# Optimization experiments

Hardware: AMD Instinct MI355X
Metric: run time of the kernel (lower is better)

The kernel has to match this reference:

```python
import jax, jax.numpy as jnp
import numpy as np

D_MODEL = 2048
N_HEADS = 16
D_K = D_MODEL // N_HEADS  # 128


def setup_inputs() -> dict:
    key = jax.random.key(0)
    ks = jax.random.split(key, 12)
    B, S = 2, 2048
    std = 1.0 / np.sqrt(D_MODEL)
    inp = {
        "query": jax.random.normal(ks[0], (B, S, D_MODEL), jnp.float32),
        "key": jax.random.normal(ks[1], (B, S, D_MODEL), jnp.float32),
        "value": jax.random.normal(ks[2], (B, S, D_MODEL), jnp.float32),
        "w_q": jax.random.normal(ks[3], (D_MODEL, D_MODEL), jnp.float32) * std,
        "b_q": jnp.zeros((D_MODEL,), jnp.float32),
        "w_k": jax.random.normal(ks[4], (D_MODEL, D_MODEL), jnp.float32) * std,
        "b_k": jnp.zeros((D_MODEL,), jnp.float32),
        "w_v": jax.random.normal(ks[5], (D_MODEL, D_MODEL), jnp.float32) * std,
        "b_v": jnp.zeros((D_MODEL,), jnp.float32),
        "w_o": jax.random.normal(ks[6], (D_MODEL, D_MODEL), jnp.float32) * std,
        "b_o": jnp.zeros((D_MODEL,), jnp.float32),
        # fractional scale numerator / denominator per head; ratio ~ 1/sqrt(d_k)
        "scale_alpha": jnp.full((N_HEADS,), 1.0, jnp.float32),
        "scale_beta": jnp.full((N_HEADS,), float(np.sqrt(D_K)), jnp.float32),
    }
    return inp


def reference(query, key, value, w_q, b_q, w_k, b_k, w_v, b_v, w_o, b_o,
              scale_alpha, scale_beta):
    B, S, _ = query.shape
    # projections (torch Linear: x @ W^T + b)
    Q = (query @ w_q.T + b_q).reshape(B, S, N_HEADS, D_K).transpose(0, 2, 1, 3)
    K = (key @ w_k.T + b_k).reshape(B, S, N_HEADS, D_K).transpose(0, 2, 1, 3)
    V = (value @ w_v.T + b_v).reshape(B, S, N_HEADS, D_K).transpose(0, 2, 1, 3)
    # per-head fractional scale alpha/beta (computed under no_grad in torch)
    scales = jax.lax.stop_gradient(scale_alpha / jnp.maximum(scale_beta, 1.0))
    scores = jnp.einsum("bhqd,bhkd->bhqk", Q, K) * scales[None, :, None, None]
    attn = jax.nn.softmax(scores, axis=-1)  # dropout is identity in eval
    out = jnp.einsum("bhqk,bhkd->bhqd", attn, V)
    out = out.transpose(0, 2, 1, 3).reshape(B, S, D_MODEL)
    return out @ w_o.T + b_o
```

## Files before the change

kernel.cpp:

```cpp
#include <hip/hip_runtime.h>
#include <cstdint>

#define S_LEN   2048
#define DMODEL  2048
#define NHEADS  16
#define DK      128
#define MROWS   4096

typedef _Float16 f16;
using f16x8 = __attribute__((ext_vector_type(8))) _Float16;
using f16x4 = __attribute__((ext_vector_type(4))) _Float16;
using f32x4 = __attribute__((ext_vector_type(4))) float;

typedef const __attribute__((address_space(1))) unsigned int gu32;
typedef __attribute__((address_space(3))) unsigned int lu32;

__device__ __forceinline__ void gl2lds16(const void* g, void* l) {
    __builtin_amdgcn_global_load_lds((gu32*)g, (lu32*)l, 16, 0, 0);
}

__global__ __launch_bounds__(256) void cvt_all(
    const float* __restrict__ q, const float* __restrict__ k,
    const float* __restrict__ v, const float* __restrict__ wq,
    const float* __restrict__ wk, const float* __restrict__ wv,
    const float* __restrict__ wo,
    f16* cq, f16* ck, f16* cv, f16* cwq, f16* cwk, f16* cwv, f16* cwo)
{
    const int b = blockIdx.x;
    const float* src; f16* dst; int base;
    if      (b <  8192) { src = q;  dst = cq;  base = b; }
    else if (b < 16384) { src = k;  dst = ck;  base = b - 8192; }
    else if (b < 24576) { src = v;  dst = cv;  base = b - 16384; }
    else if (b < 28672) { src = wq; dst = cwq; base = b - 24576; }
    else if (b < 32768) { src = wk; dst = cwk; base = b - 28672; }
    else if (b < 36864) { src = wv; dst = cwv; base = b - 32768; }
    else                { src = wo; dst = cwo; base = b - 36864; }
    const int i = base * 256 + threadIdx.x;
    float4 x = ((const float4*)src)[i];
    f16x4 o; o[0] = (f16)x.x; o[1] = (f16)x.y; o[2] = (f16)x.z; o[3] = (f16)x.w;
    ((f16x4*)dst)[i] = o;
}

__device__ __forceinline__ void gemm_core(
    const f16* __restrict__ A, const f16* __restrict__ W,
    const float* __restrict__ bias, void* __restrict__ Cout,
    int mode, const float* __restrict__ sa, const float* __restrict__ sb)
{
    __shared__ f16 As[128 * 32];
    __shared__ f16 Bs[128 * 32];

    const int tid = threadIdx.x;
    const int bm = blockIdx.y * 128;
    const int bn = blockIdx.x * 128;
    const int wid = tid >> 6;
    const int ln = tid & 15;
    const int quad = (tid & 63) >> 4;
    const int wm = (wid >> 1) * 64;
    const int wn = (wid & 1) * 64;
    const int K = DMODEL, N = DMODEL;

    f32x4 acc[4][4];
#pragma unroll
    for (int i = 0; i < 4; ++i)
#pragma unroll
        for (int j = 0; j < 4; ++j)
            acc[i][j] = (f32x4){0.f, 0.f, 0.f, 0.f};

    const int sr = tid >> 2;
    const int ke = (tid & 3) * 8;
    const f16* ga0 = A + (size_t)(bm + sr) * K + ke;
    const f16* ga1 = A + (size_t)(bm + 64 + sr) * K + ke;
    const f16* gb0 = W + (size_t)(bn + sr) * K + ke;
    const f16* gb1 = W + (size_t)(bn + 64 + sr) * K + ke;
    f16* la0 = As + tid * 8;
    f16* la1 = As + 2048 + tid * 8;
    f16* lb0 = Bs + tid * 8;
    f16* lb1 = Bs + 2048 + tid * 8;

    for (int k0 = 0; k0 < K; k0 += 32) {
        __syncthreads();
        gl2lds16(ga0 + k0, la0);
        gl2lds16(ga1 + k0, la1);
        gl2lds16(gb0 + k0, lb0);
        gl2lds16(gb1 + k0, lb1);
        __syncthreads();

        f16x8 af[4], bf[4];
#pragma unroll
        for (int i = 0; i < 4; ++i)
            af[i] = *(const f16x8*)&As[(wm + i * 16 + ln) * 32 + quad * 8];
#pragma unroll
        for (int j = 0; j < 4; ++j)
            bf[j] = *(const f16x8*)&Bs[(wn + j * 16 + ln) * 32 + quad * 8];
#pragma unroll
        for (int i = 0; i < 4; ++i)
#pragma unroll
            for (int j = 0; j < 4; ++j)
                acc[i][j] = __builtin_amdgcn_mfma_f32_16x16x32_f16(
                    af[i], bf[j], acc[i][j], 0, 0, 0);
    }

#pragma unroll
    for (int j = 0; j < 4; ++j) {
        const int n = bn + wn + j * 16 + ln;
        const float bn_ = bias[n];
        const int h = n >> 7;
        const int d = n & (DK - 1);
        float scq = 1.0f;
        if (mode == 3) scq = sa[h] / fmaxf(sb[h], 1.0f);
#pragma unroll
        for (int i = 0; i < 4; ++i) {
#pragma unroll
            for (int reg = 0; reg < 4; ++reg) {
                const int m = bm + wm + i * 16 + quad * 4 + reg;
                float v = acc[i][j][reg] + bn_;
                if (mode == 0) {
                    ((float*)Cout)[(size_t)m * N + n] = v;
                } else {
                    const int bb = m >> 11;
                    const int ss = m & (S_LEN - 1);
                    size_t idx;
                    if (mode == 2)
                        idx = (((size_t)(bb * NHEADS + h) * DK + d) * S_LEN + ss);
                    else
                        idx = (((size_t)(bb * NHEADS + h) * S_LEN + ss) * DK + d);
                    if (mode == 3) v *= scq;
                    ((f16*)Cout)[idx] = (f16)v;
                }
            }
        }
    }
}

__global__ __launch_bounds__(256) void qkv_gemm(
    const f16* Aq, const f16* Ak, const f16* Av,
    const f16* Wq, const f16* Wk, const f16* Wv,
    const float* bq, const float* bk, const float* bv,
    f16* Oq, f16* Ok, f16* Ov, const float* sa, const float* sb)
{
    const int z = blockIdx.z;
    const f16* A = (z == 0) ? Aq : (z == 1) ? Ak : Av;
    const f16* W = (z == 0) ? Wq : (z == 1) ? Wk : Wv;
    const float* bias = (z == 0) ? bq : (z == 1) ? bk : bv;
    void* O = (z == 0) ? (void*)Oq : (z == 1) ? (void*)Ok : (void*)Ov;
    const int mode = (z == 0) ? 3 : (z == 1) ? 1 : 2;
    gemm_core(A, W, bias, O, mode, sa, sb);
}

__global__ __launch_bounds__(256) void out_gemm(
    const f16* A, const f16* W, const float* bias, float* O)
{
    gemm_core(A, W, bias, O, 0, nullptr, nullptr);
}

__global__ __launch_bounds__(256, 2) void flash_v4(
    const f16* __restrict__ Qg, const f16* __restrict__ Kg,
    const f16* __restrict__ VTg, f16* __restrict__ AO)
{
    __shared__ f16 Ks[4 * 64 * 32];
    __shared__ f16 Vs[2 * 128 * 32];
    __shared__ f16 Ps[2 * 128 * 32];
    __shared__ float l_buf[2 * 128];

    const int tid = threadIdx.x;
    const int wid = tid >> 6;
    const int ln = tid & 15;
    const int quad = (tid & 63) >> 4;
    const int wq = wid & 1;
    const int wc = wid >> 1;
    const int bh = blockIdx.y;
    const int q0 = blockIdx.x * 128;

    f16x8 qf[4][4];
    const f16* Qbase = Qg + ((size_t)bh * S_LEN + q0 + wq * 64) * DK;
#pragma unroll
    for (int nt = 0; nt < 4; ++nt)
#pragma unroll
        for (int kc = 0; kc < 4; ++kc)
            qf[nt][kc] = *(const f16x8*)(Qbase + (size_t)(nt * 16 + ln) * DK
                                         + kc * 32 + quad * 8);

    f32x4 o[4][4];
    float lp[4] = {0.f, 0.f, 0.f, 0.f};
#pragma unroll
    for (int i = 0; i < 4; ++i)
#pragma unroll
        for (int j = 0; j < 4; ++j)
            o[i][j] = (f32x4){0.f, 0.f, 0.f, 0.f};

    const f16* Kgb = Kg + (size_t)bh * S_LEN * DK;
    const f16* Vgb = VTg + (size_t)bh * DK * S_LEN;
    const int srow = tid >> 2;
    const int soff = (tid & 3) * 8;

    for (int kt = 0; kt < S_LEN / 64; ++kt) {
        __syncthreads();
#pragma unroll
        for (int j = 0; j < 4; ++j)
            gl2lds16(Kgb + (size_t)(kt * 64 + srow) * DK + j * 32 + soff,
                     Ks + j * 2048 + tid * 8);
#pragma unroll
        for (int j = 0; j < 4; ++j)
            gl2lds16(Vgb + (size_t)(srow + (j & 1) * 64) * S_LEN
                         + kt * 64 + (j >> 1) * 32 + soff,
                     Vs + (j >> 1) * 4096 + (j & 1) * 2048 + tid * 8);
        __syncthreads();

        f32x4 s[2][4];
#pragma unroll
        for (int mt = 0; mt < 2; ++mt)
#pragma unroll
            for (int nt = 0; nt < 4; ++nt)
                s[mt][nt] = (f32x4){0.f, 0.f, 0.f, 0.f};
#pragma unroll
        for (int kc = 0; kc < 4; ++kc) {
            f16x8 kf0 = *(const f16x8*)&Ks[kc * 2048 + (wc * 32 + ln) * 32 + quad * 8];
            f16x8 kf1 = *(const f16x8*)&Ks[kc * 2048 + (wc * 32 + 16 + ln) * 32 + quad * 8];
#pragma unroll
            for (int nt = 0; nt < 4; ++nt) {
                s[0][nt] = __builtin_amdgcn_mfma_f32_16x16x32_f16(kf0, qf[nt][kc], s[0][nt], 0, 0, 0);
                s[1][nt] = __builtin_amdgcn_mfma_f32_16x16x32_f16(kf1, qf[nt][kc], s[1][nt], 0, 0, 0);
            }
        }

#pragma unroll
        for (int mt = 0; mt < 2; ++mt) {
#pragma unroll
            for (int nt = 0; nt < 4; ++nt) {
                const float p0 = __expf(s[mt][nt][0]);
                const float p1 = __expf(s[mt][nt][1]);
                const float p2 = __expf(s[mt][nt][2]);
                const float p3 = __expf(s[mt][nt][3]);
                lp[nt] += (p0 + p1) + (p2 + p3);
                f16x4 pk;
                pk[0] = (f16)p0; pk[1] = (f16)p1; pk[2] = (f16)p2; pk[3] = (f16)p3;
                *(f16x4*)&Ps[wc * 4096 + (wq * 64 + nt * 16 + ln) * 32
                             + mt * 16 + quad * 4] = pk;
            }
        }
        __syncthreads();

#pragma unroll
        for (int cc = 0; cc < 2; ++cc) {
            f16x8 pf[4];
#pragma unroll
            for (int mtq = 0; mtq < 4; ++mtq)
                pf[mtq] = *(const f16x8*)&Ps[cc * 4096 + (wq * 64 + mtq * 16 + ln) * 32 + quad * 8];
#pragma unroll
            for (int ntd = 0; ntd < 4; ++ntd) {
                f16x8 vf = *(const f16x8*)&Vs[cc * 4096 + (wc * 64 + ntd * 16 + ln) * 32 + quad * 8];
#pragma unroll
                for (int mtq = 0; mtq < 4; ++mtq)
                    o[mtq][ntd] = __builtin_amdgcn_mfma_f32_16x16x32_f16(
                        pf[mtq], vf, o[mtq][ntd], 0, 0, 0);
            }
        }
    }

#pragma unroll
    for (int nt = 0; nt < 4; ++nt) {
        float v = lp[nt];
        v += __shfl_xor(v, 16, 64);
        v += __shfl_xor(v, 32, 64);
        lp[nt] = v;
    }
    if (quad == 0) {
#pragma unroll
        for (int nt = 0; nt < 4; ++nt)
            l_buf[wc * 128 + wq * 64 + nt * 16 + ln] = lp[nt];
    }
    __syncthreads();

    const int b = bh >> 4;
    const int h = bh & (NHEADS - 1);
#pragma unroll
    for (int mtq = 0; mtq < 4; ++mtq) {
#pragma unroll
        for (int reg = 0; reg < 4; ++reg) {
            const int ql = wq * 64 + mtq * 16 + quad * 4 + reg;
            const float inv = 1.0f / (l_buf[ql] + l_buf[128 + ql]);
            f16* dst = AO + ((size_t)b * S_LEN + q0 + ql) * DMODEL + h * DK + wc * 64;
#pragma unroll
            for (int ntd = 0; ntd < 4; ++ntd)
                dst[ntd * 16 + ln] = (f16)(o[mtq][ntd][reg] * inv);
        }
    }
}

extern "C" void kernel_launch(void* const* d_in, const int* in_sizes, int n_in,
                              void* d_out, int out_size, void* d_ws, size_t ws_size,
                              hipStream_t stream)
{
    (void)in_sizes; (void)n_in; (void)out_size; (void)ws_size;
    const float* query = (const float*)d_in[0];
    const float* key_  = (const float*)d_in[1];
    const float* value = (const float*)d_in[2];
    const float* w_q = (const float*)d_in[3];
    const float* b_q = (const float*)d_in[4];
    const float* w_k = (const float*)d_in[5];
    const float* b_k = (const float*)d_in[6];
    const float* w_v = (const float*)d_in[7];
    const float* b_v = (const float*)d_in[8];
    const float* w_o = (const float*)d_in[9];
    const float* b_o = (const float*)d_in[10];
    const float* s_alpha = (const float*)d_in[11];
    const float* s_beta  = (const float*)d_in[12];
    float* out = (float*)d_out;

    const size_t T = (size_t)MROWS * DMODEL;
    const size_t Wn = (size_t)DMODEL * DMODEL;
    f16* base = (f16*)d_ws;
    f16* c_q = base;
    f16* c_k = base + T;
    f16* c_v = base + 2 * T;
    f16* Qh  = base + 3 * T;
    f16* wq16 = base + 4 * T;
    f16* wk16 = wq16 + Wn;
    f16* wv16 = wk16 + Wn;
    f16* wo16 = wv16 + Wn;
    f16* Kh  = c_q;
    f16* VT  = c_k;
    f16* AOh = c_v;

    dim3 blk(256);

    cvt_all<<<dim3(40960), blk, 0, stream>>>(query, key_, value, w_q, w_k, w_v, w_o,
                                             c_q, c_k, c_v, wq16, wk16, wv16, wo16);

    dim3 qkv_grid(DMODEL / 128, MROWS / 128, 3);
    qkv_gemm<<<qkv_grid, blk, 0, stream>>>(c_q, c_k, c_v, wq16, wk16, wv16,
                                           b_q, b_k, b_v, Qh, Kh, VT,
                                           s_alpha, s_beta);

    dim3 flash_grid(S_LEN / 128, 2 * NHEADS);
    flash_v4<<<flash_grid, blk, 0, stream>>>(Qh, Kh, VT, AOh);

    dim3 out_grid(DMODEL / 128, MROWS / 128);
    out_gemm<<<out_grid, blk, 0, stream>>>(AOh, wo16, b_o, out);
}
```

Before: 489.1 us.

## Triple-buffer GEMM with swizzled LDS, 128x256 tiles, and grid-stride conversion

The projection GEMMs move to 512-thread blocks with 128x256 tiles and a three-stage LDS ring. Global-to-LDS loads for tile t+2 are issued while MFMAs on tile t run, gated by vmcnt waits and raw barriers, and the compute phases get raised wave priority. An XOR swizzle on the K-chunk offset is meant to reduce LDS bank conflicts. The fp32-to-fp16 conversion kernel becomes a grid-stride loop over 2048 blocks instead of one block per chunk. The larger tiles and buffers raise LDS and register use and halve the block count, which may reduce occupancy. The hand-counted vmcnt synchronization is fragile.

```diff
diff --git a/kernel.cpp b/kernel.cpp
--- a/kernel.cpp
+++ b/kernel.cpp
@@ -19,6 +19,7 @@
     __builtin_amdgcn_global_load_lds((gu32*)g, (lu32*)l, 16, 0, 0);
 }
 
+#define CVT_BLOCKS 2048
 __global__ __launch_bounds__(256) void cvt_all(
     const float* __restrict__ q, const float* __restrict__ k,
     const float* __restrict__ v, const float* __restrict__ wq,
@@ -26,37 +27,44 @@
     const float* __restrict__ wo,
     f16* cq, f16* ck, f16* cv, f16* cwq, f16* cwk, f16* cwv, f16* cwo)
 {
-    const int b = blockIdx.x;
-    const float* src; f16* dst; int base;
-    if      (b <  8192) { src = q;  dst = cq;  base = b; }
-    else if (b < 16384) { src = k;  dst = ck;  base = b - 8192; }
-    else if (b < 24576) { src = v;  dst = cv;  base = b - 16384; }
-    else if (b < 28672) { src = wq; dst = cwq; base = b - 24576; }
-    else if (b < 32768) { src = wk; dst = cwk; base = b - 28672; }
-    else if (b < 36864) { src = wv; dst = cwv; base = b - 32768; }
-    else                { src = wo; dst = cwo; base = b - 36864; }
-    const int i = base * 256 + threadIdx.x;
-    float4 x = ((const float4*)src)[i];
-    f16x4 o; o[0] = (f16)x.x; o[1] = (f16)x.y; o[2] = (f16)x.z; o[3] = (f16)x.w;
-    ((f16x4*)dst)[i] = o;
-}
+    const unsigned QS = 2097152u;
+    const unsigned WS = 1048576u;
+    const unsigned total = 3u * QS + 4u * WS;
+    unsigned i = blockIdx.x * 256 + threadIdx.x;
+    const unsigned stride = CVT_BLOCKS * 256;
+    for (; i < total; i += stride) {
+        const float* src; f16* dst; unsigned off;
+        if      (i < QS)              { src = q;  dst = cq;  off = i; }
+        else if (i < 2u*QS)           { src = k;  dst = ck;  off = i - QS; }
+        else if (i < 3u*QS)           { src = v;  dst = cv;  off = i - 2u*QS; }
+        else if (i < 3u*QS + WS)      { src = wq; dst = cwq; off = i - 3u*QS; }
+        else if (i < 3u*QS + 2u*WS)   { src = wk; dst = cwk; off = i - (3u*QS + WS); }
+        else if (i < 3u*QS + 3u*WS)   { src = wv; dst = cwv; off = i - (3u*QS + 2u*WS); }
+        else                          { src = wo; dst = cwo; off = i - (3u*QS + 3u*WS); }
+        float4 x = ((const float4*)src)[off];
+        f16x4 o; o[0] = (f16)x.x; o[1] = (f16)x.y; o[2] = (f16)x.z; o[3] = (f16)x.w;
+        ((f16x4*)dst)[off] = o;
+    }
+}
+
+#define NT_K (DMODEL / 32)
 
 __device__ __forceinline__ void gemm_core(
     const f16* __restrict__ A, const f16* __restrict__ W,
     const float* __restrict__ bias, void* __restrict__ Cout,
     int mode, const float* __restrict__ sa, const float* __restrict__ sb)
 {
-    __shared__ f16 As[128 * 32];
-    __shared__ f16 Bs[128 * 32];
+    __shared__ f16 As[3][128 * 32];
+    __shared__ f16 Bs[3][256 * 32];
 
     const int tid = threadIdx.x;
-    const int bm = blockIdx.y * 128;
-    const int bn = blockIdx.x * 128;
     const int wid = tid >> 6;
     const int ln = tid & 15;
     const int quad = (tid & 63) >> 4;
-    const int wm = (wid >> 1) * 64;
-    const int wn = (wid & 1) * 64;
+    const int wm = (wid >> 2) * 64;
+    const int wn = (wid & 3) * 64;
+    const int bm = blockIdx.y * 128;
+    const int bn = blockIdx.x * 256;
     const int K = DMODEL, N = DMODEL;
 
     f32x4 acc[4][4];
@@ -67,37 +75,67 @@
             acc[i][j] = (f32x4){0.f, 0.f, 0.f, 0.f};
 
     const int sr = tid >> 2;
-    const int ke = (tid & 3) * 8;
-    const f16* ga0 = A + (size_t)(bm + sr) * K + ke;
-    const f16* ga1 = A + (size_t)(bm + 64 + sr) * K + ke;
-    const f16* gb0 = W + (size_t)(bn + sr) * K + ke;
-    const f16* gb1 = W + (size_t)(bn + 64 + sr) * K + ke;
-    f16* la0 = As + tid * 8;
-    f16* la1 = As + 2048 + tid * 8;
-    f16* lb0 = Bs + tid * 8;
-    f16* lb1 = Bs + 2048 + tid * 8;
-
-    for (int k0 = 0; k0 < K; k0 += 32) {
-        __syncthreads();
-        gl2lds16(ga0 + k0, la0);
-        gl2lds16(ga1 + k0, la1);
-        gl2lds16(gb0 + k0, lb0);
-        gl2lds16(gb1 + k0, lb1);
-        __syncthreads();
-
-        f16x8 af[4], bf[4];
-#pragma unroll
-        for (int i = 0; i < 4; ++i)
-            af[i] = *(const f16x8*)&As[(wm + i * 16 + ln) * 32 + quad * 8];
-#pragma unroll
-        for (int j = 0; j < 4; ++j)
-            bf[j] = *(const f16x8*)&Bs[(wn + j * 16 + ln) * 32 + quad * 8];
-#pragma unroll
-        for (int i = 0; i < 4; ++i)
+    const int kcs = ((tid & 3) ^ ((tid >> 3) & 3)) * 8;
+    const f16* gA  = A + (size_t)(bm + sr) * K + kcs;
+    const f16* gB0 = W + (size_t)(bn + sr) * K + kcs;
+    const f16* gB1 = W + (size_t)(bn + 128 + sr) * K + kcs;
+    const int koff = (quad ^ ((ln >> 1) & 3)) * 8;
+
+    gl2lds16(gA,        &As[0][tid * 8]);
+    gl2lds16(gB0,       &Bs[0][tid * 8]);
+    gl2lds16(gB1,       &Bs[0][4096 + tid * 8]);
+    gl2lds16(gA  + 32,  &As[1][tid * 8]);
+    gl2lds16(gB0 + 32,  &Bs[1][tid * 8]);
+    gl2lds16(gB1 + 32,  &Bs[1][4096 + tid * 8]);
+
+    for (int t = 0; t < NT_K; ++t) {
+        const f16* Ab = As[t % 3];
+        const f16* Bb = Bs[t % 3];
+        if (t < NT_K - 1) asm volatile("s_waitcnt vmcnt(3)" ::: "memory");
+        else              asm volatile("s_waitcnt vmcnt(0)" ::: "memory");
+        __builtin_amdgcn_s_barrier();
+
+        f16x8 af[2], bf[4];
+#pragma unroll
+        for (int i = 0; i < 2; ++i)
+            af[i] = *(const f16x8*)&Ab[(wm + i * 16 + ln) * 32 + koff];
+#pragma unroll
+        for (int j = 0; j < 4; ++j)
+            bf[j] = *(const f16x8*)&Bb[(wn + j * 16 + ln) * 32 + koff];
+        if (t + 2 < NT_K) {
+            const int b2 = (t + 2) % 3;
+            const int k2 = (t + 2) * 32;
+            gl2lds16(gA  + k2, &As[b2][tid * 8]);
+            gl2lds16(gB0 + k2, &Bs[b2][tid * 8]);
+        }
+        __builtin_amdgcn_s_barrier();
+        __builtin_amdgcn_s_setprio(1);
+#pragma unroll
+        for (int i = 0; i < 2; ++i)
 #pragma unroll
             for (int j = 0; j < 4; ++j)
                 acc[i][j] = __builtin_amdgcn_mfma_f32_16x16x32_f16(
                     af[i], bf[j], acc[i][j], 0, 0, 0);
+        __builtin_amdgcn_s_setprio(0);
+        __builtin_amdgcn_s_barrier();
+
+#pragma unroll
+        for (int i = 0; i < 2; ++i)
+            af[i] = *(const f16x8*)&Ab[(wm + (2 + i) * 16 + ln) * 32 + koff];
+        if (t + 2 < NT_K) {
+            const int b2 = (t + 2) % 3;
+            const int k2 = (t + 2) * 32;
+            gl2lds16(gB1 + k2, &Bs[b2][4096 + tid * 8]);
+        }
+        __builtin_amdgcn_s_barrier();
+        __builtin_amdgcn_s_setprio(1);
+#pragma unroll
+        for (int i = 0; i < 2; ++i)
+#pragma unroll
+            for (int j = 0; j < 4; ++j)
+                acc[2 + i][j] = __builtin_amdgcn_mfma_f32_16x16x32_f16(
+                    af[i], bf[j], acc[2 + i][j], 0, 0, 0);
+        __builtin_amdgcn_s_setprio(0);
     }
 
 #pragma unroll
@@ -132,7 +170,7 @@
     }
 }
 
-__global__ __launch_bounds__(256) void qkv_gemm(
+__global__ __launch_bounds__(512, 2) void qkv_gemm(
     const f16* Aq, const f16* Ak, const f16* Av,
     const f16* Wq, const f16* Wk, const f16* Wv,
     const float* bq, const float* bk, const float* bv,
@@ -147,7 +185,7 @@
     gemm_core(A, W, bias, O, mode, sa, sb);
 }
 
-__global__ __launch_bounds__(256) void out_gemm(
+__global__ __launch_bounds__(512, 2) void out_gemm(
     const f16* A, const f16* W, const float* bias, float* O)
 {
     gemm_core(A, W, bias, O, 0, nullptr, nullptr);
@@ -322,19 +360,18 @@
     f16* VT  = c_k;
     f16* AOh = c_v;
 
-    dim3 blk(256);
-
-    cvt_all<<<dim3(40960), blk, 0, stream>>>(query, key_, value, w_q, w_k, w_v, w_o,
-                                             c_q, c_k, c_v, wq16, wk16, wv16, wo16);
-
-    dim3 qkv_grid(DMODEL / 128, MROWS / 128, 3);
-    qkv_gemm<<<qkv_grid, blk, 0, stream>>>(c_q, c_k, c_v, wq16, wk16, wv16,
-                                           b_q, b_k, b_v, Qh, Kh, VT,
-                                           s_alpha, s_beta);
+    cvt_all<<<dim3(CVT_BLOCKS), dim3(256), 0, stream>>>(
+        query, key_, value, w_q, w_k, w_v, w_o,
+        c_q, c_k, c_v, wq16, wk16, wv16, wo16);
+
+    dim3 qkv_grid(DMODEL / 256, MROWS / 128, 3);
+    qkv_gemm<<<qkv_grid, dim3(512), 0, stream>>>(c_q, c_k, c_v, wq16, wk16, wv16,
+                                                 b_q, b_k, b_v, Qh, Kh, VT,
+                                                 s_alpha, s_beta);
 
     dim3 flash_grid(S_LEN / 128, 2 * NHEADS);
-    flash_v4<<<flash_grid, blk, 0, stream>>>(Qh, Kh, VT, AOh);
-
-    dim3 out_grid(DMODEL / 128, MROWS / 128);
-    out_gemm<<<out_grid, blk, 0, stream>>>(AOh, wo16, b_o, out);
-}
+    flash_v4<<<flash_grid, dim3(256), 0, stream>>>(Qh, Kh, VT, AOh);
+
+    dim3 out_grid(DMODEL / 256, MROWS / 128);
+    out_gemm<<<out_grid, dim3(512), 0, stream>>>(AOh, wo16, b_o, out);
+}
```

Measured after the change: 498.2 us. Within noise of the previous version (+1.9%).

## Use 256-row GEMM tiles with 4-stage async LDS pipeline and swizzled LDS

Applied to the files above, without the earlier changes.

Replaces the 128x128 single-buffered GEMM with 512-thread blocks computing 256x256 tiles (QKV) or 256x128 tiles (output projection). Global-to-LDS loads now run through a 4-deep ring buffer with explicit vmcnt waits and MFMA priority raising. Both the GEMM and the flash-attention K, V and P tiles get an XOR swizzle on the LDS layout to avoid bank conflicts. K and V^T are moved into the output buffer so the QKV GEMM no longer overwrites its own input buffers while other blocks still read them. The larger tiles and deeper buffering use more LDS and registers, which may limit occupancy.

```diff
diff --git a/kernel.cpp b/kernel.cpp
--- a/kernel.cpp
+++ b/kernel.cpp
@@ -41,67 +41,108 @@
     ((f16x4*)dst)[i] = o;
 }
 
-__device__ __forceinline__ void gemm_core(
+#define NT_K (DMODEL / 32)
+
+template<int BN>
+__device__ __forceinline__ void gemm_core2(
     const f16* __restrict__ A, const f16* __restrict__ W,
     const float* __restrict__ bias, void* __restrict__ Cout,
     int mode, const float* __restrict__ sa, const float* __restrict__ sb)
 {
-    __shared__ f16 As[128 * 32];
-    __shared__ f16 Bs[128 * 32];
-
-    const int tid = threadIdx.x;
-    const int bm = blockIdx.y * 128;
-    const int bn = blockIdx.x * 128;
-    const int wid = tid >> 6;
-    const int ln = tid & 15;
+    constexpr int NJ = BN / 64;
+    __shared__ f16 As[4][256 * 32];
+    __shared__ f16 Bs[4][BN * 32];
+
+    const int tid  = threadIdx.x;
+    const int wid  = tid >> 6;
+    const int ln   = tid & 15;
     const int quad = (tid & 63) >> 4;
-    const int wm = (wid >> 1) * 64;
-    const int wn = (wid & 1) * 64;
+    const int wm   = (wid >> 2) * 128;
+    const int wn   = (wid & 3) * (16 * NJ);
+    const int bm   = blockIdx.y * 256;
+    const int bn   = blockIdx.x * BN;
     const int K = DMODEL, N = DMODEL;
 
-    f32x4 acc[4][4];
-#pragma unroll
-    for (int i = 0; i < 4; ++i)
-#pragma unroll
-        for (int j = 0; j < 4; ++j)
+    f32x4 acc[8][NJ];
+#pragma unroll
+    for (int i = 0; i < 8; ++i)
+#pragma unroll
+        for (int j = 0; j < NJ; ++j)
             acc[i][j] = (f32x4){0.f, 0.f, 0.f, 0.f};
 
-    const int sr = tid >> 2;
-    const int ke = (tid & 3) * 8;
-    const f16* ga0 = A + (size_t)(bm + sr) * K + ke;
-    const f16* ga1 = A + (size_t)(bm + 64 + sr) * K + ke;
-    const f16* gb0 = W + (size_t)(bn + sr) * K + ke;
-    const f16* gb1 = W + (size_t)(bn + 64 + sr) * K + ke;
-    f16* la0 = As + tid * 8;
-    f16* la1 = As + 2048 + tid * 8;
-    f16* lb0 = Bs + tid * 8;
-    f16* lb1 = Bs + 2048 + tid * 8;
-
-    for (int k0 = 0; k0 < K; k0 += 32) {
-        __syncthreads();
-        gl2lds16(ga0 + k0, la0);
-        gl2lds16(ga1 + k0, la1);
-        gl2lds16(gb0 + k0, lb0);
-        gl2lds16(gb1 + k0, lb1);
-        __syncthreads();
-
-        f16x8 af[4], bf[4];
+    const int sr  = tid >> 2;
+    const int kcs = ((tid & 3) ^ ((tid >> 3) & 3)) * 8;
+    const f16* gA0 = A + (size_t)(bm + sr) * K + kcs;
+    const f16* gA1 = A + (size_t)(bm + 128 + sr) * K + kcs;
+    const f16* gB0 = W + (size_t)(bn + sr) * K + kcs;
+    const f16* gB1 = W + (size_t)(bn + 128 + sr) * K + kcs;
+    const int koff = (quad ^ ((ln >> 1) & 3)) * 8;
+
+#define STAGE_A(t_) do { const int b_ = (t_) & 3; const int k_ = (t_) * 32; \
+        gl2lds16(gA0 + k_, &As[b_][tid * 8]);                               \
+        gl2lds16(gA1 + k_, &As[b_][4096 + tid * 8]); } while (0)
+#define STAGE_B(t_) do { const int b_ = (t_) & 3; const int k_ = (t_) * 32; \
+        gl2lds16(gB0 + k_, &Bs[b_][tid * 8]);                               \
+        if (BN == 256) gl2lds16(gB1 + k_, &Bs[b_][4096 + tid * 8]); } while (0)
+
+    STAGE_A(0); STAGE_B(0);
+    STAGE_A(1); STAGE_B(1);
+    STAGE_A(2); STAGE_B(2);
+
+    for (int t = 0; t < NT_K; ++t) {
+        const f16* Ab = As[t & 3];
+        const f16* Bb = Bs[t & 3];
+        if (BN == 256) {
+            if (t < NT_K - 2)       asm volatile("s_waitcnt vmcnt(8)" ::: "memory");
+            else if (t == NT_K - 2) asm volatile("s_waitcnt vmcnt(4)" ::: "memory");
+            else                    asm volatile("s_waitcnt vmcnt(0)" ::: "memory");
+        } else {
+            if (t < NT_K - 2)       asm volatile("s_waitcnt vmcnt(6)" ::: "memory");
+            else if (t == NT_K - 2) asm volatile("s_waitcnt vmcnt(3)" ::: "memory");
+            else                    asm volatile("s_waitcnt vmcnt(0)" ::: "memory");
+        }
+        __builtin_amdgcn_s_barrier();
+        __builtin_amdgcn_sched_barrier(0);
+
+        f16x8 af[4], bf[NJ];
 #pragma unroll
         for (int i = 0; i < 4; ++i)
-            af[i] = *(const f16x8*)&As[(wm + i * 16 + ln) * 32 + quad * 8];
-#pragma unroll
-        for (int j = 0; j < 4; ++j)
-            bf[j] = *(const f16x8*)&Bs[(wn + j * 16 + ln) * 32 + quad * 8];
+            af[i] = *(const f16x8*)&Ab[(wm + i * 16 + ln) * 32 + koff];
+#pragma unroll
+        for (int j = 0; j < NJ; ++j)
+            bf[j] = *(const f16x8*)&Bb[(wn + j * 16 + ln) * 32 + koff];
+        if (t + 3 < NT_K) STAGE_A(t + 3);
+        asm volatile("s_waitcnt lgkmcnt(0)" ::: "memory");
+        __builtin_amdgcn_sched_barrier(0);
+        __builtin_amdgcn_s_setprio(1);
 #pragma unroll
         for (int i = 0; i < 4; ++i)
 #pragma unroll
-            for (int j = 0; j < 4; ++j)
+            for (int j = 0; j < NJ; ++j)
                 acc[i][j] = __builtin_amdgcn_mfma_f32_16x16x32_f16(
                     af[i], bf[j], acc[i][j], 0, 0, 0);
-    }
-
-#pragma unroll
-    for (int j = 0; j < 4; ++j) {
+        __builtin_amdgcn_s_setprio(0);
+
+#pragma unroll
+        for (int i = 0; i < 4; ++i)
+            af[i] = *(const f16x8*)&Ab[(wm + (4 + i) * 16 + ln) * 32 + koff];
+        if (t + 3 < NT_K) STAGE_B(t + 3);
+        asm volatile("s_waitcnt lgkmcnt(0)" ::: "memory");
+        __builtin_amdgcn_sched_barrier(0);
+        __builtin_amdgcn_s_setprio(1);
+#pragma unroll
+        for (int i = 0; i < 4; ++i)
+#pragma unroll
+            for (int j = 0; j < NJ; ++j)
+                acc[4 + i][j] = __builtin_amdgcn_mfma_f32_16x16x32_f16(
+                    af[i], bf[j], acc[4 + i][j], 0, 0, 0);
+        __builtin_amdgcn_s_setprio(0);
+    }
+#undef STAGE_A
+#undef STAGE_B
+
+#pragma unroll
+    for (int j = 0; j < NJ; ++j) {
         const int n = bn + wn + j * 16 + ln;
         const float bn_ = bias[n];
         const int h = n >> 7;
@@ -109,7 +150,7 @@
         float scq = 1.0f;
         if (mode == 3) scq = sa[h] / fmaxf(sb[h], 1.0f);
 #pragma unroll
-        for (int i = 0; i < 4; ++i) {
+        for (int i = 0; i < 8; ++i) {
 #pragma unroll
             for (int reg = 0; reg < 4; ++reg) {
                 const int m = bm + wm + i * 16 + quad * 4 + reg;
@@ -132,7 +173,7 @@
     }
 }
 
-__global__ __launch_bounds__(256) void qkv_gemm(
+__global__ __launch_bounds__(512, 2) void qkv_gemm(
     const f16* Aq, const f16* Ak, const f16* Av,
     const f16* Wq, const f16* Wk, const f16* Wv,
     const float* bq, const float* bk, const float* bv,
@@ -144,13 +185,13 @@
     const float* bias = (z == 0) ? bq : (z == 1) ? bk : bv;
     void* O = (z == 0) ? (void*)Oq : (z == 1) ? (void*)Ok : (void*)Ov;
     const int mode = (z == 0) ? 3 : (z == 1) ? 1 : 2;
-    gemm_core(A, W, bias, O, mode, sa, sb);
-}
-
-__global__ __launch_bounds__(256) void out_gemm(
+    gemm_core2<256>(A, W, bias, O, mode, sa, sb);
+}
+
+__global__ __launch_bounds__(512, 2) void out_gemm(
     const f16* A, const f16* W, const float* bias, float* O)
 {
-    gemm_core(A, W, bias, O, 0, nullptr, nullptr);
+    gemm_core2<128>(A, W, bias, O, 0, nullptr, nullptr);
 }
 
 __global__ __launch_bounds__(256, 2) void flash_v4(
@@ -171,6 +212,9 @@
     const int bh = blockIdx.y;
     const int q0 = blockIdx.x * 128;
 
+    const int koff = (quad ^ ((ln >> 1) & 3)) * 8;
+    const int soff_sw = ((tid & 3) ^ ((tid >> 3) & 3)) * 8;
+
     f16x8 qf[4][4];
     const f16* Qbase = Qg + ((size_t)bh * S_LEN + q0 + wq * 64) * DK;
 #pragma unroll
@@ -191,18 +235,17 @@
     const f16* Kgb = Kg + (size_t)bh * S_LEN * DK;
     const f16* Vgb = VTg + (size_t)bh * DK * S_LEN;
     const int srow = tid >> 2;
-    const int soff = (tid & 3) * 8;
 
     for (int kt = 0; kt < S_LEN / 64; ++kt) {
         __syncthreads();
 #pragma unroll
         for (int j = 0; j < 4; ++j)
-            gl2lds16(Kgb + (size_t)(kt * 64 + srow) * DK + j * 32 + soff,
+            gl2lds16(Kgb + (size_t)(kt * 64 + srow) * DK + j * 32 + soff_sw,
                      Ks + j * 2048 + tid * 8);
 #pragma unroll
         for (int j = 0; j < 4; ++j)
             gl2lds16(Vgb + (size_t)(srow + (j & 1) * 64) * S_LEN
-                         + kt * 64 + (j >> 1) * 32 + soff,
+                         + kt * 64 + (j >> 1) * 32 + soff_sw,
                      Vs + (j >> 1) * 4096 + (j & 1) * 2048 + tid * 8);
         __syncthreads();
 
@@ -212,16 +255,18 @@
 #pragma unroll
             for (int nt = 0; nt < 4; ++nt)
                 s[mt][nt] = (f32x4){0.f, 0.f, 0.f, 0.f};
+        __builtin_amdgcn_s_setprio(1);
 #pragma unroll
         for (int kc = 0; kc < 4; ++kc) {
-            f16x8 kf0 = *(const f16x8*)&Ks[kc * 2048 + (wc * 32 + ln) * 32 + quad * 8];
-            f16x8 kf1 = *(const f16x8*)&Ks[kc * 2048 + (wc * 32 + 16 + ln) * 32 + quad * 8];
+            f16x8 kf0 = *(const f16x8*)&Ks[kc * 2048 + (wc * 32 + ln) * 32 + koff];
+            f16x8 kf1 = *(const f16x8*)&Ks[kc * 2048 + (wc * 32 + 16 + ln) * 32 + koff];
 #pragma unroll
             for (int nt = 0; nt < 4; ++nt) {
                 s[0][nt] = __builtin_amdgcn_mfma_f32_16x16x32_f16(kf0, qf[nt][kc], s[0][nt], 0, 0, 0);
                 s[1][nt] = __builtin_amdgcn_mfma_f32_16x16x32_f16(kf1, qf[nt][kc], s[1][nt], 0, 0, 0);
             }
         }
+        __builtin_amdgcn_s_setprio(0);
 
 #pragma unroll
         for (int mt = 0; mt < 2; ++mt) {
@@ -234,27 +279,30 @@
                 lp[nt] += (p0 + p1) + (p2 + p3);
                 f16x4 pk;
                 pk[0] = (f16)p0; pk[1] = (f16)p1; pk[2] = (f16)p2; pk[3] = (f16)p3;
-                *(f16x4*)&Ps[wc * 4096 + (wq * 64 + nt * 16 + ln) * 32
-                             + mt * 16 + quad * 4] = pk;
+                const int pchunk = ((mt * 2 + (quad >> 1)) ^ ((ln >> 1) & 3)) * 8
+                                   + (quad & 1) * 4;
+                *(f16x4*)&Ps[wc * 4096 + (wq * 64 + nt * 16 + ln) * 32 + pchunk] = pk;
             }
         }
         __syncthreads();
 
+        __builtin_amdgcn_s_setprio(1);
 #pragma unroll
         for (int cc = 0; cc < 2; ++cc) {
             f16x8 pf[4];
 #pragma unroll
             for (int mtq = 0; mtq < 4; ++mtq)
-                pf[mtq] = *(const f16x8*)&Ps[cc * 4096 + (wq * 64 + mtq * 16 + ln) * 32 + quad * 8];
+                pf[mtq] = *(const f16x8*)&Ps[cc * 4096 + (wq * 64 + mtq * 16 + ln) * 32 + koff];
 #pragma unroll
             for (int ntd = 0; ntd < 4; ++ntd) {
-                f16x8 vf = *(const f16x8*)&Vs[cc * 4096 + (wc * 64 + ntd * 16 + ln) * 32 + quad * 8];
+                f16x8 vf = *(const f16x8*)&Vs[cc * 4096 + (wc * 64 + ntd * 16 + ln) * 32 + koff];
 #pragma unroll
                 for (int mtq = 0; mtq < 4; ++mtq)
                     o[mtq][ntd] = __builtin_amdgcn_mfma_f32_16x16x32_f16(
                         pf[mtq], vf, o[mtq][ntd], 0, 0, 0);
             }
         }
+        __builtin_amdgcn_s_setprio(0);
     }
 
 #pragma unroll
@@ -318,23 +366,22 @@
     f16* wk16 = wq16 + Wn;
     f16* wv16 = wk16 + Wn;
     f16* wo16 = wv16 + Wn;
-    f16* Kh  = c_q;
-    f16* VT  = c_k;
+    f16* Kh  = (f16*)d_out;
+    f16* VT  = Kh + T;
     f16* AOh = c_v;
 
-    dim3 blk(256);
-
-    cvt_all<<<dim3(40960), blk, 0, stream>>>(query, key_, value, w_q, w_k, w_v, w_o,
-                                             c_q, c_k, c_v, wq16, wk16, wv16, wo16);
-
-    dim3 qkv_grid(DMODEL / 128, MROWS / 128, 3);
-    qkv_gemm<<<qkv_grid, blk, 0, stream>>>(c_q, c_k, c_v, wq16, wk16, wv16,
-                                           b_q, b_k, b_v, Qh, Kh, VT,
-                                           s_alpha, s_beta);
+    cvt_all<<<dim3(40960), dim3(256), 0, stream>>>(
+        query, key_, value, w_q, w_k, w_v, w_o,
+        c_q, c_k, c_v, wq16, wk16, wv16, wo16);
+
+    dim3 qkv_grid(DMODEL / 256, MROWS / 256, 3);
+    qkv_gemm<<<qkv_grid, dim3(512), 0, stream>>>(c_q, c_k, c_v, wq16, wk16, wv16,
+                                                 b_q, b_k, b_v, Qh, Kh, VT,
+                                                 s_alpha, s_beta);
 
     dim3 flash_grid(S_LEN / 128, 2 * NHEADS);
-    flash_v4<<<flash_grid, blk, 0, stream>>>(Qh, Kh, VT, AOh);
-
-    dim3 out_grid(DMODEL / 128, MROWS / 128);
-    out_gemm<<<out_grid, blk, 0, stream>>>(AOh, wo16, b_o, out);
-}
+    flash_v4<<<flash_grid, dim3(256), 0, stream>>>(Qh, Kh, VT, AOh);
+
+    dim3 out_grid(DMODEL / 128, MROWS / 256);
+    out_gemm<<<out_grid, dim3(512), 0, stream>>>(AOh, wo16, b_o, out);
+}
```

Measured after the change: 484.3 us. About the same (-1.0%).

## Double-buffer K tiles, swizzle LDS layouts, and remap blocks in flash attention

Applied to the files above, without the earlier changes.

The flash kernel now double-buffers K tiles in LDS: the next K tile is prefetched while the current scores and softmax are computed, and explicit waitcnt plus s_barrier replace the full __syncthreads. K, V and P in LDS use an XOR-swizzled chunk layout to reduce bank conflicts. Block indices are remapped to group work for better L2 locality, and s_setprio is raised around the MFMA sections. The fp32-to-fp16 conversion kernel does four vectors per thread. K and V^T scratch moves into the output buffer, which also removes aliasing with the converted query that qkv_gemm is still reading. The hand-written wait counts are fragile if the load order ever changes.

```diff
diff --git a/kernel.cpp b/kernel.cpp
--- a/kernel.cpp
+++ b/kernel.cpp
@@ -28,17 +28,20 @@
 {
     const int b = blockIdx.x;
     const float* src; f16* dst; int base;
-    if      (b <  8192) { src = q;  dst = cq;  base = b; }
-    else if (b < 16384) { src = k;  dst = ck;  base = b - 8192; }
-    else if (b < 24576) { src = v;  dst = cv;  base = b - 16384; }
-    else if (b < 28672) { src = wq; dst = cwq; base = b - 24576; }
-    else if (b < 32768) { src = wk; dst = cwk; base = b - 28672; }
-    else if (b < 36864) { src = wv; dst = cwv; base = b - 32768; }
-    else                { src = wo; dst = cwo; base = b - 36864; }
-    const int i = base * 256 + threadIdx.x;
-    float4 x = ((const float4*)src)[i];
-    f16x4 o; o[0] = (f16)x.x; o[1] = (f16)x.y; o[2] = (f16)x.z; o[3] = (f16)x.w;
-    ((f16x4*)dst)[i] = o;
+    if      (b <  2048) { src = q;  dst = cq;  base = b; }
+    else if (b <  4096) { src = k;  dst = ck;  base = b - 2048; }
+    else if (b <  6144) { src = v;  dst = cv;  base = b - 4096; }
+    else if (b <  7168) { src = wq; dst = cwq; base = b - 6144; }
+    else if (b <  8192) { src = wk; dst = cwk; base = b - 7168; }
+    else if (b <  9216) { src = wv; dst = cwv; base = b - 8192; }
+    else                { src = wo; dst = cwo; base = b - 9216; }
+    const int i = base * 1024 + threadIdx.x;
+#pragma unroll
+    for (int u = 0; u < 4; ++u) {
+        float4 x = ((const float4*)src)[i + u * 256];
+        f16x4 o; o[0] = (f16)x.x; o[1] = (f16)x.y; o[2] = (f16)x.z; o[3] = (f16)x.w;
+        ((f16x4*)dst)[i + u * 256] = o;
+    }
 }
 
 __device__ __forceinline__ void gemm_core(
@@ -153,11 +156,11 @@
     gemm_core(A, W, bias, O, 0, nullptr, nullptr);
 }
 
-__global__ __launch_bounds__(256, 2) void flash_v4(
+__global__ __launch_bounds__(256, 2) void flash_v6(
     const f16* __restrict__ Qg, const f16* __restrict__ Kg,
     const f16* __restrict__ VTg, f16* __restrict__ AO)
 {
-    __shared__ f16 Ks[4 * 64 * 32];
+    __shared__ f16 Ks[2][4 * 64 * 32];
     __shared__ f16 Vs[2 * 128 * 32];
     __shared__ f16 Ps[2 * 128 * 32];
     __shared__ float l_buf[2 * 128];
@@ -168,8 +171,14 @@
     const int quad = (tid & 63) >> 4;
     const int wq = wid & 1;
     const int wc = wid >> 1;
-    const int bh = blockIdx.y;
-    const int q0 = blockIdx.x * 128;
+
+    const int lin = blockIdx.x + (blockIdx.y << 4);
+    const int swz = (lin & 7) * 64 + (lin >> 3);
+    const int q0 = (swz & 15) * 128;
+    const int bh = swz >> 4;
+
+    const int koff = (quad ^ ((ln >> 1) & 3)) * 8;
+    const int soff_sw = ((tid & 3) ^ ((tid >> 3) & 3)) * 8;
 
     f16x8 qf[4][4];
     const f16* Qbase = Qg + ((size_t)bh * S_LEN + q0 + wq * 64) * DK;
@@ -191,36 +200,52 @@
     const f16* Kgb = Kg + (size_t)bh * S_LEN * DK;
     const f16* Vgb = VTg + (size_t)bh * DK * S_LEN;
     const int srow = tid >> 2;
-    const int soff = (tid & 3) * 8;
+
+#pragma unroll
+    for (int j = 0; j < 4; ++j)
+        gl2lds16(Kgb + (size_t)(srow)*DK + j * 32 + soff_sw,
+                 &Ks[0][j * 2048 + tid * 8]);
 
     for (int kt = 0; kt < S_LEN / 64; ++kt) {
-        __syncthreads();
-#pragma unroll
-        for (int j = 0; j < 4; ++j)
-            gl2lds16(Kgb + (size_t)(kt * 64 + srow) * DK + j * 32 + soff,
-                     Ks + j * 2048 + tid * 8);
+        asm volatile("s_waitcnt lgkmcnt(0)" ::: "memory");
+        __builtin_amdgcn_s_barrier();
+        __builtin_amdgcn_sched_barrier(0);
+
 #pragma unroll
         for (int j = 0; j < 4; ++j)
             gl2lds16(Vgb + (size_t)(srow + (j & 1) * 64) * S_LEN
-                         + kt * 64 + (j >> 1) * 32 + soff,
+                         + kt * 64 + (j >> 1) * 32 + soff_sw,
                      Vs + (j >> 1) * 4096 + (j & 1) * 2048 + tid * 8);
-        __syncthreads();
-
+
+        asm volatile("s_waitcnt vmcnt(4)" ::: "memory");
+        __builtin_amdgcn_s_barrier();
+        __builtin_amdgcn_sched_barrier(0);
+
+        const f16* Kb = &Ks[kt & 1][0];
         f32x4 s[2][4];
 #pragma unroll
         for (int mt = 0; mt < 2; ++mt)
 #pragma unroll
             for (int nt = 0; nt < 4; ++nt)
                 s[mt][nt] = (f32x4){0.f, 0.f, 0.f, 0.f};
+        __builtin_amdgcn_s_setprio(1);
 #pragma unroll
         for (int kc = 0; kc < 4; ++kc) {
-            f16x8 kf0 = *(const f16x8*)&Ks[kc * 2048 + (wc * 32 + ln) * 32 + quad * 8];
-            f16x8 kf1 = *(const f16x8*)&Ks[kc * 2048 + (wc * 32 + 16 + ln) * 32 + quad * 8];
+            f16x8 kf0 = *(const f16x8*)&Kb[kc * 2048 + (wc * 32 + ln) * 32 + koff];
+            f16x8 kf1 = *(const f16x8*)&Kb[kc * 2048 + (wc * 32 + 16 + ln) * 32 + koff];
 #pragma unroll
             for (int nt = 0; nt < 4; ++nt) {
                 s[0][nt] = __builtin_amdgcn_mfma_f32_16x16x32_f16(kf0, qf[nt][kc], s[0][nt], 0, 0, 0);
                 s[1][nt] = __builtin_amdgcn_mfma_f32_16x16x32_f16(kf1, qf[nt][kc], s[1][nt], 0, 0, 0);
             }
+        }
+        __builtin_amdgcn_s_setprio(0);
+
+        if (kt + 1 < S_LEN / 64) {
+#pragma unroll
+            for (int j = 0; j < 4; ++j)
+                gl2lds16(Kgb + (size_t)((kt + 1) * 64 + srow) * DK + j * 32 + soff_sw,
+                         &Ks[(kt + 1) & 1][j * 2048 + tid * 8]);
         }
 
 #pragma unroll
@@ -234,27 +259,35 @@
                 lp[nt] += (p0 + p1) + (p2 + p3);
                 f16x4 pk;
                 pk[0] = (f16)p0; pk[1] = (f16)p1; pk[2] = (f16)p2; pk[3] = (f16)p3;
-                *(f16x4*)&Ps[wc * 4096 + (wq * 64 + nt * 16 + ln) * 32
-                             + mt * 16 + quad * 4] = pk;
+                const int pchunk = ((mt * 2 + (quad >> 1)) ^ ((ln >> 1) & 3)) * 8
+                                   + (quad & 1) * 4;
+                *(f16x4*)&Ps[wc * 4096 + (wq * 64 + nt * 16 + ln) * 32 + pchunk] = pk;
             }
         }
-        __syncthreads();
-
+
+        if (kt + 1 < S_LEN / 64) asm volatile("s_waitcnt vmcnt(4)" ::: "memory");
+        else                     asm volatile("s_waitcnt vmcnt(0)" ::: "memory");
+        asm volatile("s_waitcnt lgkmcnt(0)" ::: "memory");
+        __builtin_amdgcn_s_barrier();
+        __builtin_amdgcn_sched_barrier(0);
+
+        __builtin_amdgcn_s_setprio(1);
 #pragma unroll
         for (int cc = 0; cc < 2; ++cc) {
             f16x8 pf[4];
 #pragma unroll
             for (int mtq = 0; mtq < 4; ++mtq)
-                pf[mtq] = *(const f16x8*)&Ps[cc * 4096 + (wq * 64 + mtq * 16 + ln) * 32 + quad * 8];
+                pf[mtq] = *(const f16x8*)&Ps[cc * 4096 + (wq * 64 + mtq * 16 + ln) * 32 + koff];
 #pragma unroll
             for (int ntd = 0; ntd < 4; ++ntd) {
-                f16x8 vf = *(const f16x8*)&Vs[cc * 4096 + (wc * 64 + ntd * 16 + ln) * 32 + quad * 8];
+                f16x8 vf = *(const f16x8*)&Vs[cc * 4096 + (wc * 64 + ntd * 16 + ln) * 32 + koff];
 #pragma unroll
                 for (int mtq = 0; mtq < 4; ++mtq)
                     o[mtq][ntd] = __builtin_amdgcn_mfma_f32_16x16x32_f16(
                         pf[mtq], vf, o[mtq][ntd], 0, 0, 0);
             }
         }
+        __builtin_amdgcn_s_setprio(0);
     }
 
 #pragma unroll
@@ -264,6 +297,7 @@
         v += __shfl_xor(v, 32, 64);
         lp[nt] = v;
     }
+    __syncthreads();
     if (quad == 0) {
 #pragma unroll
         for (int nt = 0; nt < 4; ++nt)
@@ -318,23 +352,22 @@
     f16* wk16 = wq16 + Wn;
     f16* wv16 = wk16 + Wn;
     f16* wo16 = wv16 + Wn;
-    f16* Kh  = c_q;
-    f16* VT  = c_k;
+    f16* Kh  = (f16*)d_out;
+    f16* VT  = Kh + T;
     f16* AOh = c_v;
 
-    dim3 blk(256);
-
-    cvt_all<<<dim3(40960), blk, 0, stream>>>(query, key_, value, w_q, w_k, w_v, w_o,
-                                             c_q, c_k, c_v, wq16, wk16, wv16, wo16);
+    cvt_all<<<dim3(10240), dim3(256), 0, stream>>>(
+        query, key_, value, w_q, w_k, w_v, w_o,
+        c_q, c_k, c_v, wq16, wk16, wv16, wo16);
 
     dim3 qkv_grid(DMODEL / 128, MROWS / 128, 3);
-    qkv_gemm<<<qkv_grid, blk, 0, stream>>>(c_q, c_k, c_v, wq16, wk16, wv16,
-                                           b_q, b_k, b_v, Qh, Kh, VT,
-                                           s_alpha, s_beta);
+    qkv_gemm<<<qkv_grid, dim3(256), 0, stream>>>(c_q, c_k, c_v, wq16, wk16, wv16,
+                                                 b_q, b_k, b_v, Qh, Kh, VT,
+                                                 s_alpha, s_beta);
 
     dim3 flash_grid(S_LEN / 128, 2 * NHEADS);
-    flash_v4<<<flash_grid, blk, 0, stream>>>(Qh, Kh, VT, AOh);
+    flash_v6<<<flash_grid, dim3(256), 0, stream>>>(Qh, Kh, VT, AOh);
 
     dim3 out_grid(DMODEL / 128, MROWS / 128);
-    out_gemm<<<out_grid, blk, 0, stream>>>(AOh, wo16, b_o, out);
-}
+    out_gemm<<<out_grid, dim3(256), 0, stream>>>(AOh, wo16, b_o, out);
+}
```

New measurement: 460.4 us. -5.9%, faster.
